# Performance work log

Measured on AMD Instinct MI355X. Metric: run time of the kernel, lower is better.

Reference implementation:

```python
import jax, jax.numpy as jnp
import numpy as np

NUM_AGENTS = 5
B = 512          # graphs in batch
NP = 50          # nodes per graph
N = B * NP
EPG = 400        # edges per graph
E = B * EPG
H, C = 8, 64     # heads, per-head channels
F = H * C        # 512 node feature dim after concat
GRU_IN = 2 * F   # agent emb + graph emb
GRU_H = 128


def _gat_layer(x, src, dst, ea, W, a_src, a_dst, We, ae, b):
    # PyG GATConv: per-edge additive attention with edge features, softmax over dst
    n = x.shape[0]
    h = (x @ W).reshape(n, H, C)                          # [n,H,C]
    al = (h * a_src).sum(-1)[src] + (h * a_dst).sum(-1)[dst] \
         + ((ea @ We).reshape(-1, H, C) * ae).sum(-1)     # [e,H]
    al = jax.nn.leaky_relu(al, 0.2)
    amax = jax.ops.segment_max(al, dst, num_segments=n)
    amax = jnp.where(jnp.isfinite(amax), amax, 0.0)
    p = jnp.exp(al - amax[dst])
    denom = jax.ops.segment_sum(p, dst, num_segments=n)
    alpha = p / (denom[dst] + 1e-16)
    out = jax.ops.segment_sum(alpha[:, :, None] * h[src], dst, num_segments=n)
    return out.reshape(n, F) + b


def _gru(x_seq, h0, Wih, Whh, bih, bhh):
    # torch nn.GRU math, batch_first input [B,T,I]
    def step(h, x_t):
        gi = x_t @ Wih + bih
        gh = h @ Whh + bhh
        ir, iz, inn = jnp.split(gi, 3, axis=-1)
        hr, hz, hn = jnp.split(gh, 3, axis=-1)
        r = jax.nn.sigmoid(ir + hr)
        z = jax.nn.sigmoid(iz + hz)
        n_ = jnp.tanh(inn + r * hn)
        h_new = (1.0 - z) * n_ + z * h
        return h_new, h_new
    h_last, ys = jax.lax.scan(step, h0, jnp.swapaxes(x_seq, 0, 1))
    return jnp.swapaxes(ys, 0, 1), h_last


def _forward(x, edge_index, edge_attr, hidden_state,
             W1, a_src1, a_dst1, We1, ae1, b1,
             W2, a_src2, a_dst2, We2, ae2, b2,
             W3, a_src3, a_dst3, We3, ae3, b3,
             gru_Wih, gru_Whh, gru_bih, gru_bhh,
             fc1_W, fc1_b, fc2_W, fc2_b, log_std):
    src, dst = edge_index[0], edge_index[1]
    # conv1: add_self_loops=False
    x1 = jax.nn.relu(_gat_layer(x, src, dst, edge_attr, W1, a_src1, a_dst1, We1, ae1, b1))
    # conv2/3: add self loops with fill_value='mean' (mean of incoming edge_attr per node)
    cnt = jax.ops.segment_sum(jnp.ones((E,), x.dtype), dst, num_segments=N)
    loop_attr = jax.ops.segment_sum(edge_attr, dst, num_segments=N) / jnp.maximum(cnt, 1.0)[:, None]
    loops = jnp.arange(N, dtype=edge_index.dtype)
    src2 = jnp.concatenate([src, loops])
    dst2 = jnp.concatenate([dst, loops])
    ea2 = jnp.concatenate([edge_attr, loop_attr], axis=0)
    x2 = jax.nn.relu(_gat_layer(x1, src2, dst2, ea2, W2, a_src2, a_dst2, We2, ae2, b2))
    x3 = jax.nn.relu(_gat_layer(x2, src2, dst2, ea2, W3, a_src3, a_dst3, We3, ae3, b3))
    # global mean pool (each graph has NP nodes, contiguous)
    batch = jnp.repeat(jnp.arange(B), NP)
    graph_emb = jax.ops.segment_sum(x3, batch, num_segments=B) / NP   # [B,F]
    # first NUM_AGENTS nodes of each graph
    agent_idx = (jnp.arange(B)[:, None] * NP + jnp.arange(NUM_AGENTS)).reshape(-1)
    agent_emb = x3[agent_idx]                                          # [B*A,F]
    graph_rep = jnp.repeat(graph_emb, NUM_AGENTS, axis=0)
    combined = jnp.concatenate([agent_emb, graph_rep], axis=1).reshape(B, NUM_AGENTS, GRU_IN)
    gru_out, h_last = _gru(combined, hidden_state[0], gru_Wih, gru_Whh, gru_bih, gru_bhh)
    f1 = jax.nn.relu(gru_out.reshape(-1, GRU_H) @ fc1_W + fc1_b)
    action_mean = (f1 @ fc2_W + fc2_b).reshape(B, NUM_AGENTS, -1)
    action_std = jnp.broadcast_to(jnp.exp(jnp.clip(log_std, -20.0, 2.0)), action_mean.shape)
    return action_mean, action_std, h_last[None]


def setup_inputs() -> dict:
    ks = jax.random.split(jax.random.key(0), 24)
    rng = np.random.default_rng(0)
    # random edges within each graph, no self-loops
    src_l = rng.integers(0, NP, size=(B, EPG))
    dst_l = (src_l + 1 + rng.integers(0, NP - 1, size=(B, EPG))) % NP
    off = (np.arange(B) * NP)[:, None]
    edge_index = jnp.asarray(np.stack([(src_l + off).reshape(-1), (dst_l + off).reshape(-1)]), dtype=jnp.int32)

    def p(k, shape, fan):
        return jax.random.normal(k, shape, jnp.float32) / float(np.sqrt(fan))

    z = lambda *s: jnp.zeros(s, jnp.float32)
    return {
        "x": jax.random.normal(ks[0], (N, 4), jnp.float32),
        "edge_index": edge_index,
        "edge_attr": jax.random.uniform(ks[1], (E, 1), jnp.float32),
        "hidden_state": z(1, B, GRU_H),
        "W1": p(ks[2], (4, F), 4), "a_src1": p(ks[3], (H, C), C), "a_dst1": p(ks[4], (H, C), C),
        "We1": p(ks[5], (1, F), 1), "ae1": p(ks[6], (H, C), C), "b1": z(F),
        "W2": p(ks[7], (F, F), F), "a_src2": p(ks[8], (H, C), C), "a_dst2": p(ks[9], (H, C), C),
        "We2": p(ks[10], (1, F), 1), "ae2": p(ks[11], (H, C), C), "b2": z(F),
        "W3": p(ks[12], (F, F), F), "a_src3": p(ks[13], (H, C), C), "a_dst3": p(ks[14], (H, C), C),
        "We3": p(ks[15], (1, F), 1), "ae3": p(ks[16], (H, C), C), "b3": z(F),
        "gru_Wih": p(ks[17], (GRU_IN, 3 * GRU_H), GRU_IN),
        "gru_Whh": p(ks[18], (GRU_H, 3 * GRU_H), GRU_H),
        "gru_bih": z(3 * GRU_H), "gru_bhh": z(3 * GRU_H),
        "fc1_W": p(ks[19], (GRU_H, 64), GRU_H), "fc1_b": z(64),
        "fc2_W": p(ks[20], (64, 3), 64), "fc2_b": z(3),
        "log_std": jnp.full((1, 1, 3), -1.6, jnp.float32),
    }


def reference(x, edge_index, edge_attr, hidden_state,
              W1, a_src1, a_dst1, We1, ae1, b1,
              W2, a_src2, a_dst2, We2, ae2, b2,
              W3, a_src3, a_dst3, We3, ae3, b3,
              gru_Wih, gru_Whh, gru_bih, gru_bhh,
              fc1_W, fc1_b, fc2_W, fc2_b, log_std):
    return _forward(x, edge_index, edge_attr, hidden_state,
                    W1, a_src1, a_dst1, We1, ae1, b1,
                    W2, a_src2, a_dst2, We2, ae2, b2,
                    W3, a_src3, a_dst3, We3, ae3, b3,
                    gru_Wih, gru_Whh, gru_bih, gru_bhh,
                    fc1_W, fc1_b, fc2_W, fc2_b, log_std)
```

## Files before the change

kernel.cpp:

```cpp
#include <hip/hip_runtime.h>
#include <math.h>

#define NN 25600
#define BB 512
#define NP 50
#define EPG 400
#define EE 204800
#define HH 8
#define FF 512
#define GRUH 128
#define GRUIN 1024

typedef unsigned short ushort_t;
typedef __attribute__((ext_vector_type(8))) short bf16x8;
typedef __attribute__((ext_vector_type(4))) float f32x4;

__device__ __forceinline__ float wave_reduce_sum(float v) {
  #pragma unroll
  for (int m = 32; m >= 1; m >>= 1) v += __shfl_xor(v, m, 64);
  return v;
}

__device__ __forceinline__ ushort_t f2bf(float x) {
  union { float f; unsigned int u; } v; v.f = x;
  unsigned int r = v.u + 0x7fffu + ((v.u >> 16) & 1u);
  return (ushort_t)(r >> 16);
}

__device__ __forceinline__ float bf2f(ushort_t u) {
  union { unsigned int u; float f; } v; v.u = ((unsigned int)u) << 16;
  return v.f;
}

__device__ __forceinline__ void gload_lds16(const ushort_t* g, ushort_t* l) {
  __builtin_amdgcn_global_load_lds(
      (const __attribute__((address_space(1))) void*)g,
      (__attribute__((address_space(3))) void*)l, 16, 0, 0);
}

__global__ __launch_bounds__(256) void k_pre(
    const float* __restrict__ W2, const float* __restrict__ W3,
    const float* __restrict__ Wih,
    ushort_t* __restrict__ w2t, ushort_t* __restrict__ w3t, ushort_t* __restrict__ wiht,
    const int* __restrict__ ei, const float* __restrict__ eattr,
    int* __restrict__ rowp, ushort_t* __restrict__ esrc, float* __restrict__ eea,
    float* __restrict__ lattr,
    const float* __restrict__ We1, const float* __restrict__ ae1,
    const float* __restrict__ We2, const float* __restrict__ ae2,
    const float* __restrict__ We3, const float* __restrict__ ae3,
    float* __restrict__ wdot) {
  int b = blockIdx.x, tid = threadIdx.x;
  __shared__ float t[32][33];
  __shared__ int cnt[NP];
  __shared__ float esum[NP];
  __shared__ int rp[NP + 1];
  __shared__ int cur[NP];

  if (b < 896) {
    const float* W; ushort_t* Wt; int K, N, n0, k0;
    if (b < 256)      { W = W2;  Wt = w2t;  K = 512;  N = 512; n0 = (b & 15) * 32;        k0 = (b >> 4) * 32; }
    else if (b < 512) { W = W3;  Wt = w3t;  K = 512;  N = 512; n0 = ((b - 256) & 15) * 32; k0 = ((b - 256) >> 4) * 32; }
    else              { W = Wih; Wt = wiht; K = 1024; N = 384; n0 = ((b - 512) % 12) * 32; k0 = ((b - 512) / 12) * 32; }
    int tx = tid & 31, ty = tid >> 5;
    #pragma unroll
    for (int i = 0; i < 4; i++)
      t[ty + i * 8][tx] = W[(size_t)(k0 + ty + i * 8) * N + n0 + tx];
    __syncthreads();
    #pragma unroll
    for (int i = 0; i < 4; i++)
      Wt[(size_t)(n0 + ty + i * 8) * K + k0 + tx] = f2bf(t[tx][ty + i * 8]);
  } else if (b < 1408) {
    int g = b - 896;
    if (tid < NP) { cnt[tid] = 0; esum[tid] = 0.f; }
    __syncthreads();
    for (int e = tid; e < EPG; e += 256) {
      int ge = g * EPG + e;
      int dl = ei[EE + ge] - g * NP;
      atomicAdd(&cnt[dl], 1);
      atomicAdd(&esum[dl], eattr[ge]);
    }
    __syncthreads();
    if (tid == 0) {
      int s = 0;
      for (int i = 0; i < NP; i++) { rp[i] = s; cur[i] = s; s += cnt[i]; }
      rp[NP] = s;
    }
    __syncthreads();
    if (tid <= NP) rowp[g * 64 + tid] = rp[tid];
    if (tid < NP) lattr[g * NP + tid] = esum[tid] / (float)max(cnt[tid], 1);
    for (int e = tid; e < EPG; e += 256) {
      int ge = g * EPG + e;
      int sl = ei[ge] - g * NP;
      int dl = ei[EE + ge] - g * NP;
      int pos = atomicAdd(&cur[dl], 1);
      esrc[g * EPG + pos] = (ushort_t)sl;
      eea[g * EPG + pos] = eattr[ge];
    }
  } else {
    int w = tid >> 6, lane = tid & 63;
    for (int i = 0; i < 6; i++) {
      int idx = w + 4 * i;
      int l = idx >> 3, h = idx & 7;
      const float* We = l == 0 ? We1 : (l == 1 ? We2 : We3);
      const float* ae = l == 0 ? ae1 : (l == 1 ? ae2 : ae3);
      float v = wave_reduce_sum(We[h * 64 + lane] * ae[h * 64 + lane]);
      if (lane == 0) wdot[l * 8 + h] = v;
    }
  }
}

__global__ __launch_bounds__(512, 4) void k_layer(
    const ushort_t* __restrict__ Xbf,
    const float* __restrict__ x4, const float* __restrict__ W1,
    const ushort_t* __restrict__ Wt,
    const float* __restrict__ a_src, const float* __restrict__ a_dst,
    ushort_t* __restrict__ xout, ushort_t* __restrict__ cbf,
    const int* __restrict__ rowp, const ushort_t* __restrict__ esrc,
    const float* __restrict__ eea, const float* __restrict__ lattr,
    const float* __restrict__ wdot_all, const float* __restrict__ bias,
    int layer, int self_loops) {
  int g = blockIdx.x, half = blockIdx.y, tid = threadIdx.x;
  int w = tid >> 6, l = tid & 63;
  int head = w & 3, fhalf = w >> 2;
  int flb = head * 64 + fhalf * 32;
  int fbase = half * 256;
  int m_l = l & 15, quad = l >> 4, rq = quad * 4, kq8 = quad * 8;

  __shared__ __align__(16) ushort_t hS[256 * 64];
  __shared__ __align__(16) ushort_t U[12800];
  __shared__ float pds[512], pdd[512];
  __shared__ float sslS[256], sdlS[256];
  __shared__ ushort_t esrcS[400];
  __shared__ float eeaS[400];
  __shared__ int rowpS[51];
  __shared__ float lattrS[50];

  for (int i = tid; i < 400; i += 512) { esrcS[i] = esrc[g * EPG + i]; eeaS[i] = eea[g * EPG + i]; }
  if (tid <= NP) rowpS[tid] = rowp[g * 64 + tid];
  if (tid < NP) lattrS[tid] = lattr[g * NP + tid];

  f32x4 acc[2][4];
  #pragma unroll
  for (int i = 0; i < 2; i++)
    #pragma unroll
    for (int j = 0; j < 4; j++) acc[i][j] = (f32x4){0.f, 0.f, 0.f, 0.f};

  if (layer == 0) {
    float* W1s = (float*)U;
    float* xs = (float*)U + 1024;
    for (int i = tid; i < 1024; i += 512)
      W1s[i] = W1[(i >> 8) * 512 + fbase + (i & 255)];
    if (tid < NP) *(float4*)(&xs[tid * 4]) = *(const float4*)(&x4[(size_t)(g * NP + tid) * 4]);
    else if (tid < 64) *(float4*)(&xs[tid * 4]) = make_float4(0.f, 0.f, 0.f, 0.f);
    __syncthreads();
    float xr[4][4];
    #pragma unroll
    for (int nt = 0; nt < 4; nt++)
      #pragma unroll
      for (int k = 0; k < 4; k++) xr[nt][k] = xs[(nt * 16 + m_l) * 4 + k];
    #pragma unroll
    for (int mt = 0; mt < 2; mt++) {
      float wv[4][4];
      #pragma unroll
      for (int r = 0; r < 4; r++)
        #pragma unroll
        for (int k = 0; k < 4; k++) wv[r][k] = W1s[k * 256 + flb + mt * 16 + rq + r];
      #pragma unroll
      for (int nt = 0; nt < 4; nt++)
        #pragma unroll
        for (int r = 0; r < 4; r++)
          acc[mt][nt][r] = xr[nt][0] * wv[r][0] + xr[nt][1] * wv[r][1]
                         + xr[nt][2] * wv[r][2] + xr[nt][3] * wv[r][3];
    }
    __syncthreads();
  } else {
    ushort_t* Bs = U;
    const ushort_t* Arow = Wt + (size_t)(fbase + flb + m_l) * FF + kq8;
    const ushort_t* Bg = Xbf + (size_t)(g * NP + w * 16 + (l >> 2)) * FF + (l & 3) * 8;
    ushort_t* BsW = U + w * 512;
    for (int k0 = 0; k0 < FF; k0 += 128) {
      if (w < 4) {
        #pragma unroll
        for (int j = 0; j < 4; j++)
          gload_lds16(Bg + k0 + j * 32, BsW + j * 2048);
      }
      __syncthreads();
      #pragma unroll
      for (int j = 0; j < 4; j++) {
        int kk = k0 + j * 32;
        bf16x8 af0 = *(const bf16x8*)(Arow + kk);
        bf16x8 af1 = *(const bf16x8*)(Arow + (size_t)16 * FF + kk);
        #pragma unroll
        for (int nt = 0; nt < 4; nt++) {
          bf16x8 bf = *(const bf16x8*)(Bs + j * 2048 + (nt * 16 + m_l) * 32 + kq8);
          acc[0][nt] = __builtin_amdgcn_mfma_f32_16x16x32_bf16(af0, bf, acc[0][nt], 0, 0, 0);
          acc[1][nt] = __builtin_amdgcn_mfma_f32_16x16x32_bf16(af1, bf, acc[1][nt], 0, 0, 0);
        }
      }
      __syncthreads();
    }
  }

  float ds[4] = {0.f, 0.f, 0.f, 0.f}, dd[4] = {0.f, 0.f, 0.f, 0.f};
  #pragma unroll
  for (int mt = 0; mt < 2; mt++) {
    float a_s[4], a_d[4];
    #pragma unroll
    for (int r = 0; r < 4; r++) {
      int fg = fbase + flb + mt * 16 + rq + r;
      a_s[r] = a_src[fg]; a_d[r] = a_dst[fg];
    }
    #pragma unroll
    for (int nt = 0; nt < 4; nt++) {
      int s = nt * 16 + m_l;
      #pragma unroll
      for (int r = 0; r < 4; r++) {
        float v = acc[mt][nt][r];
        ds[nt] += v * a_s[r];
        dd[nt] += v * a_d[r];
        int fl = flb + mt * 16 + rq + r;
        hS[fl * 64 + (s ^ (((fl >> 2) & 7) << 3))] = f2bf(v);
      }
    }
  }
  #pragma unroll
  for (int nt = 0; nt < 4; nt++) {
    ds[nt] += __shfl_xor(ds[nt], 16, 64); ds[nt] += __shfl_xor(ds[nt], 32, 64);
    dd[nt] += __shfl_xor(dd[nt], 16, 64); dd[nt] += __shfl_xor(dd[nt], 32, 64);
  }
  if (l < 16) {
    #pragma unroll
    for (int nt = 0; nt < 4; nt++) {
      pds[w * 64 + nt * 16 + l] = ds[nt];
      pdd[w * 64 + nt * 16 + l] = dd[nt];
    }
  }
  __syncthreads();

  { uint4* z = (uint4*)U; for (int i = tid; i < 1600; i += 512) z[i] = make_uint4(0u, 0u, 0u, 0u); }
  if (tid < 256) {
    sslS[tid] = pds[tid] + pds[tid + 256];
    sdlS[tid] = pdd[tid] + pdd[tid + 256];
  }
  __syncthreads();

  float wdot = wdot_all[layer * 8 + half * 4 + head];
  if (w < 4 && l < NP) {
    ushort_t* AmH = U + w * 3200;
    int d = l;
    int e0 = rowpS[d], e1 = rowpS[d + 1];
    float sd = sdlS[w * 64 + d];
    float m = -1e30f;
    for (int e = e0; e < e1; e++) {
      float al = sslS[w * 64 + esrcS[e]] + sd + eeaS[e] * wdot;
      al = al > 0.f ? al : 0.2f * al;
      m = fmaxf(m, al);
    }
    float al_loop = 0.f;
    if (self_loops) {
      al_loop = sslS[w * 64 + d] + sd + lattrS[d] * wdot;
      al_loop = al_loop > 0.f ? al_loop : 0.2f * al_loop;
      m = fmaxf(m, al_loop);
    }
    if (e1 > e0 || self_loops) {
      float denom = 0.f;
      for (int e = e0; e < e1; e++) {
        float al = sslS[w * 64 + esrcS[e]] + sd + eeaS[e] * wdot;
        al = al > 0.f ? al : 0.2f * al;
        float p = __expf(al - m);
        denom += p;
        int sp = esrcS[e] ^ ((d & 3) << 3);
        float prev = bf2f(AmH[d * 64 + sp]);
        AmH[d * 64 + sp] = f2bf(prev + p);
      }
      if (self_loops) {
        float p = __expf(al_loop - m);
        denom += p;
        int sp = d ^ ((d & 3) << 3);
        float prev = bf2f(AmH[d * 64 + sp]);
        AmH[d * 64 + sp] = f2bf(prev + p);
      }
      float inv = 1.f / (denom + 1e-16f);
      #pragma unroll
      for (int c = 0; c < 8; c++) {
        union { ushort_t u[8]; uint4 q; } pk;
        pk.q = *(uint4*)(AmH + d * 64 + c * 8);
        #pragma unroll
        for (int j = 0; j < 8; j++) pk.u[j] = f2bf(bf2f(pk.u[j]) * inv);
        *(uint4*)(AmH + d * 64 + c * 8) = pk.q;
      }
    }
  }
  __syncthreads();

  ushort_t* AmW = U + head * 3200;
  f32x4 oacc[2][4];
  #pragma unroll
  for (int i = 0; i < 2; i++)
    #pragma unroll
    for (int j = 0; j < 4; j++) oacc[i][j] = (f32x4){0.f, 0.f, 0.f, 0.f};
  #pragma unroll
  for (int kc = 0; kc < 2; kc++) {
    int kb = kc * 32 + kq8;
    bf16x8 bfr2[4];
    #pragma unroll
    for (int nt = 0; nt < 4; nt++) {
      int d = nt * 16 + m_l;
      int rd = d < NP ? d : 0;
      bfr2[nt] = *(const bf16x8*)(AmW + rd * 64 + (kb ^ ((rd & 3) << 3)));
    }
    #pragma unroll
    for (int mt = 0; mt < 2; mt++) {
      int fl = flb + mt * 16 + m_l;
      bf16x8 afr = *(const bf16x8*)(hS + fl * 64 + (kb ^ (((fl >> 2) & 7) << 3)));
      #pragma unroll
      for (int nt = 0; nt < 4; nt++)
        oacc[mt][nt] = __builtin_amdgcn_mfma_f32_16x16x32_bf16(afr, bfr2[nt], oacc[mt][nt], 0, 0, 0);
    }
  }

  float vv[2][4][4];
  #pragma unroll
  for (int mt = 0; mt < 2; mt++) {
    const float4 bv = *(const float4*)(&bias[fbase + flb + mt * 16 + rq]);
    #pragma unroll
    for (int nt = 0; nt < 4; nt++) {
      vv[mt][nt][0] = fmaxf(oacc[mt][nt][0] + bv.x, 0.f);
      vv[mt][nt][1] = fmaxf(oacc[mt][nt][1] + bv.y, 0.f);
      vv[mt][nt][2] = fmaxf(oacc[mt][nt][2] + bv.z, 0.f);
      vv[mt][nt][3] = fmaxf(oacc[mt][nt][3] + bv.w, 0.f);
    }
  }

  if (cbf == nullptr) {
    #pragma unroll
    for (int nt = 0; nt < 4; nt++) {
      int d = nt * 16 + m_l;
      if (d < NP) {
        #pragma unroll
        for (int mt = 0; mt < 2; mt++) {
          union { ushort_t u[4]; uint2 v; } pk;
          #pragma unroll
          for (int r = 0; r < 4; r++) pk.u[r] = f2bf(vv[mt][nt][r]);
          *(uint2*)(&xout[(size_t)(g * NP + d) * FF + fbase + flb + mt * 16 + rq]) = pk.v;
        }
      }
    }
  } else {
    #pragma unroll
    for (int mt = 0; mt < 2; mt++) {
      float msum[4];
      #pragma unroll
      for (int r = 0; r < 4; r++) {
        float t = 0.f;
        #pragma unroll
        for (int nt = 0; nt < 4; nt++) {
          int d = nt * 16 + m_l;
          t += (d < NP) ? vv[mt][nt][r] : 0.f;
        }
        t += __shfl_xor(t, 1, 64); t += __shfl_xor(t, 2, 64);
        t += __shfl_xor(t, 4, 64); t += __shfl_xor(t, 8, 64);
        msum[r] = t * (1.f / NP);
      }
      if (m_l == 0) {
        union { ushort_t u[4]; uint2 v; } pk;
        #pragma unroll
        for (int r = 0; r < 4; r++) pk.u[r] = f2bf(msum[r]);
        #pragma unroll
        for (int t5 = 0; t5 < 5; t5++)
          *(uint2*)(&cbf[(size_t)(g * 5 + t5) * GRUIN + 512 + fbase + flb + mt * 16 + rq]) = pk.v;
      }
      if (m_l < 5) {
        union { ushort_t u[4]; uint2 v; } pk;
        #pragma unroll
        for (int r = 0; r < 4; r++) pk.u[r] = f2bf(vv[mt][0][r]);
        *(uint2*)(&cbf[(size_t)(g * 5 + m_l) * GRUIN + fbase + flb + mt * 16 + rq]) = pk.v;
      }
    }
  }
}

__global__ __launch_bounds__(256) void k_bgemm(
    const ushort_t* __restrict__ A, const ushort_t* __restrict__ Bt,
    const float* __restrict__ bias, float* __restrict__ C,
    int M, int N, int K) {
  __shared__ ushort_t As[128 * 32];
  __shared__ ushort_t Bs[128 * 32];
  int tid = threadIdx.x;
  int w = tid >> 6, l = tid & 63;
  int row0 = blockIdx.y * 128, col0 = blockIdx.x * 128;
  int wr = w >> 1, wc = w & 1;

  f32x4 acc[4][4];
  #pragma unroll
  for (int i = 0; i < 4; i++)
    #pragma unroll
    for (int j = 0; j < 4; j++) acc[i][j] = (f32x4){0.f, 0.f, 0.f, 0.f};

  int srow = w * 32 + (l >> 2);
  int skcol = (l & 3) * 8;
  const ushort_t* Ag = A + (size_t)(row0 + srow) * K + skcol;
  const ushort_t* Bg = Bt + (size_t)(col0 + srow) * K + skcol;
  ushort_t* AsW = &As[w * 1024];
  ushort_t* BsW = &Bs[w * 1024];

  int m_l = l & 15, kq = (l >> 4) * 8;
  const ushort_t* ArdA = &As[(wr * 64 + m_l) * 32 + kq];
  const ushort_t* BrdB = &Bs[(wc * 64 + m_l) * 32 + kq];

  for (int k0 = 0; k0 < K; k0 += 32) {
    gload_lds16(Ag + k0, AsW);
    gload_lds16(Ag + (size_t)16 * K + k0, AsW + 512);
    gload_lds16(Bg + k0, BsW);
    gload_lds16(Bg + (size_t)16 * K + k0, BsW + 512);
    __syncthreads();
    bf16x8 af[4], bfr[4];
    #pragma unroll
    for (int t = 0; t < 4; t++) {
      af[t]  = *(const bf16x8*)(ArdA + t * 16 * 32);
      bfr[t] = *(const bf16x8*)(BrdB + t * 16 * 32);
    }
    #pragma unroll
    for (int mt = 0; mt < 4; mt++)
      #pragma unroll
      for (int nt = 0; nt < 4; nt++)
        acc[mt][nt] = __builtin_amdgcn_mfma_f32_16x16x32_bf16(af[mt], bfr[nt], acc[mt][nt], 0, 0, 0);
    __syncthreads();
  }

  int cl = l & 15, rq = (l >> 4) * 4;
  #pragma unroll
  for (int mt = 0; mt < 4; mt++) {
    #pragma unroll
    for (int nt = 0; nt < 4; nt++) {
      int col = col0 + wc * 64 + nt * 16 + cl;
      float bv = bias ? bias[col] : 0.f;
      #pragma unroll
      for (int r = 0; r < 4; r++) {
        int row = row0 + wr * 64 + mt * 16 + rq + r;
        C[(size_t)row * N + col] = acc[mt][nt][r] + bv;
      }
    }
  }
}

__global__ void k_grufc(const float* __restrict__ gi_all, const float* __restrict__ h0,
                        const float* __restrict__ Whh, const float* __restrict__ bhh,
                        const float* __restrict__ fc1W, const float* __restrict__ fc1b,
                        const float* __restrict__ fc2W, const float* __restrict__ fc2b,
                        const float* __restrict__ log_std, float* __restrict__ dout) {
  int b = blockIdx.x, tid = threadIdx.x;
  __shared__ float hl[GRUH];
  __shared__ float ghb[384];
  __shared__ float go[5 * GRUH];
  __shared__ float f1[5 * 64];
  if (tid < GRUH) hl[tid] = h0[b * GRUH + tid];
  for (int t = 0; t < 5; t++) {
    __syncthreads();
    float acc = bhh[tid];
    for (int k = 0; k < GRUH; k++) acc += hl[k] * Whh[k * 384 + tid];
    ghb[tid] = acc;
    __syncthreads();
    if (tid < GRUH) {
      const float* gi = gi_all + (size_t)(b * 5 + t) * 384;
      float r = 1.f / (1.f + expf(-(gi[tid] + ghb[tid])));
      float z = 1.f / (1.f + expf(-(gi[128 + tid] + ghb[128 + tid])));
      float nn = tanhf(gi[256 + tid] + r * ghb[256 + tid]);
      float hn = (1.f - z) * nn + z * hl[tid];
      go[t * GRUH + tid] = hn;
      hl[tid] = hn;
    }
  }
  __syncthreads();
  if (tid < GRUH) dout[15360 + b * GRUH + tid] = hl[tid];
  if (tid < 320) {
    int t = tid >> 6, j = tid & 63;
    float acc = fc1b[j];
    for (int k = 0; k < GRUH; k++) acc += go[t * GRUH + k] * fc1W[k * 64 + j];
    f1[t * 64 + j] = fmaxf(acc, 0.f);
  }
  __syncthreads();
  if (tid < 15) {
    int t = tid / 3, o = tid % 3;
    float v = fc2b[o];
    for (int j = 0; j < 64; j++) v += f1[t * 64 + j] * fc2W[j * 3 + o];
    dout[(b * 5 + t) * 3 + o] = v;
    float ls = log_std[o];
    ls = fminf(fmaxf(ls, -20.f), 2.f);
    dout[7680 + (b * 5 + t) * 3 + o] = expf(ls);
  }
}

extern "C" void kernel_launch(void* const* d_in, const int* in_sizes, int n_in,
                              void* d_out, int out_size, void* d_ws, size_t ws_size,
                              hipStream_t stream) {
  const float* x      = (const float*)d_in[0];
  const int*   ei     = (const int*)d_in[1];
  const float* eattr  = (const float*)d_in[2];
  const float* hstate = (const float*)d_in[3];
  const float* W1  = (const float*)d_in[4];
  const float* as1 = (const float*)d_in[5];
  const float* ad1 = (const float*)d_in[6];
  const float* We1 = (const float*)d_in[7];
  const float* ae1 = (const float*)d_in[8];
  const float* b1  = (const float*)d_in[9];
  const float* W2  = (const float*)d_in[10];
  const float* as2 = (const float*)d_in[11];
  const float* ad2 = (const float*)d_in[12];
  const float* We2 = (const float*)d_in[13];
  const float* ae2 = (const float*)d_in[14];
  const float* b2  = (const float*)d_in[15];
  const float* W3  = (const float*)d_in[16];
  const float* as3 = (const float*)d_in[17];
  const float* ad3 = (const float*)d_in[18];
  const float* We3 = (const float*)d_in[19];
  const float* ae3 = (const float*)d_in[20];
  const float* b3  = (const float*)d_in[21];
  const float* Wih = (const float*)d_in[22];
  const float* Whh = (const float*)d_in[23];
  const float* bih = (const float*)d_in[24];
  const float* bhh = (const float*)d_in[25];
  const float* fc1W = (const float*)d_in[26];
  const float* fc1b = (const float*)d_in[27];
  const float* fc2W = (const float*)d_in[28];
  const float* fc2b = (const float*)d_in[29];
  const float* lstd = (const float*)d_in[30];

  float* ws = (float*)d_ws;
  ushort_t* xbf1 = (ushort_t*)ws;
  ushort_t* xbf2 = (ushort_t*)(ws + 6569984);
  float* p = ws + 2 * 6569984;
  int*   rowp  = (int*)p;         p += 32768;
  ushort_t* esrc = (ushort_t*)p;  p += 102400;
  float* eea   = p;               p += 204800;
  float* lattr = p;               p += 25600;
  float* wdot  = p;               p += 32;
  ushort_t* w2t  = (ushort_t*)p;  p += 131072;
  ushort_t* w3t  = (ushort_t*)p;  p += 131072;
  ushort_t* wiht = (ushort_t*)p;  p += 196608;
  ushort_t* cbf  = (ushort_t*)p;  p += 1310720;
  float* gi_all  = p;             p += 983040;
  float* dout = (float*)d_out;

  k_pre<<<1409, 256, 0, stream>>>(W2, W3, Wih, w2t, w3t, wiht, ei, eattr,
                                  rowp, esrc, eea, lattr,
                                  We1, ae1, We2, ae2, We3, ae3, wdot);

  k_layer<<<dim3(BB, 2), 512, 0, stream>>>(nullptr, x, W1, nullptr, as1, ad1,
                                           xbf1, nullptr, rowp, esrc, eea, lattr,
                                           wdot, b1, 0, 0);
  k_layer<<<dim3(BB, 2), 512, 0, stream>>>(xbf1, nullptr, nullptr, w2t, as2, ad2,
                                           xbf2, nullptr, rowp, esrc, eea, lattr,
                                           wdot, b2, 1, 1);
  k_layer<<<dim3(BB, 2), 512, 0, stream>>>(xbf2, nullptr, nullptr, w3t, as3, ad3,
                                           nullptr, cbf, rowp, esrc, eea, lattr,
                                           wdot, b3, 2, 1);

  k_bgemm<<<dim3(3, 20), 256, 0, stream>>>(cbf, wiht, bih, gi_all, 2560, 384, GRUIN);

  k_grufc<<<BB, 384, 0, stream>>>(gi_all, hstate, Whh, bhh, fc1W, fc1b,
                                  fc2W, fc2b, lstd, dout);
}
```

Baseline: 318.8 us.

## Stage weight tiles in LDS for projection GEMM and pad h layout

The projection GEMM for layers 2-3 now stages both the transposed weight tile and the node-feature tile into shared memory with async global-to-LDS loads over 64-wide K chunks, using all 8 waves for loading. Previously weight fragments were read straight from global memory per lane. The h tile moves from an XOR-swizzled layout to a row-padded layout (stride 72), and the bf16 results are written as packed 32-bit pairs exchanged across neighbouring lanes. The aim is fewer scattered global reads and LDS bank conflicts, in exchange for more shared memory per block, which may lower occupancy.

Measured after the change: 319.7 us. No clear change (+0.3%).

```diff
diff --git a/kernel.cpp b/kernel.cpp
--- a/kernel.cpp
+++ b/kernel.cpp
@@ -121,13 +121,13 @@
     int layer, int self_loops) {
   int g = blockIdx.x, half = blockIdx.y, tid = threadIdx.x;
   int w = tid >> 6, l = tid & 63;
-  int head = w & 3, fhalf = w >> 2;
-  int flb = head * 64 + fhalf * 32;
+  int head = w & 3;
+  int flb = head * 64 + (w >> 2) * 32;
   int fbase = half * 256;
   int m_l = l & 15, quad = l >> 4, rq = quad * 4, kq8 = quad * 8;
 
-  __shared__ __align__(16) ushort_t hS[256 * 64];
-  __shared__ __align__(16) ushort_t U[12800];
+  __shared__ __align__(16) ushort_t hS[256 * 72];
+  __shared__ __align__(16) ushort_t AmU[12800];
   __shared__ float pds[512], pdd[512];
   __shared__ float sslS[256], sdlS[256];
   __shared__ ushort_t esrcS[400];
@@ -146,8 +146,8 @@
     for (int j = 0; j < 4; j++) acc[i][j] = (f32x4){0.f, 0.f, 0.f, 0.f};
 
   if (layer == 0) {
-    float* W1s = (float*)U;
-    float* xs = (float*)U + 1024;
+    float* W1s = (float*)AmU;
+    float* xs = (float*)AmU + 1024;
     for (int i = tid; i < 1024; i += 512)
       W1s[i] = W1[(i >> 8) * 512 + fbase + (i & 255)];
     if (tid < NP) *(float4*)(&xs[tid * 4]) = *(const float4*)(&x4[(size_t)(g * NP + tid) * 4]);
@@ -174,27 +174,29 @@
     }
     __syncthreads();
   } else {
-    ushort_t* Bs = U;
-    const ushort_t* Arow = Wt + (size_t)(fbase + flb + m_l) * FF + kq8;
-    const ushort_t* Bg = Xbf + (size_t)(g * NP + w * 16 + (l >> 2)) * FF + (l & 3) * 8;
-    ushort_t* BsW = U + w * 512;
-    for (int k0 = 0; k0 < FF; k0 += 128) {
-      if (w < 4) {
-        #pragma unroll
-        for (int j = 0; j < 4; j++)
-          gload_lds16(Bg + k0 + j * 32, BsW + j * 2048);
-      }
+    ushort_t* hA = hS;
+    ushort_t* hB = AmU;
+    int arow = (l >> 3), acol = (l & 7) * 8;
+    for (int k0 = 0; k0 < FF; k0 += 64) {
+      #pragma unroll
+      for (int j = 0; j < 4; j++)
+        gload_lds16(Wt + (size_t)(fbase + w * 32 + j * 8 + arow) * FF + k0 + acol,
+                    hA + w * 2048 + j * 512);
+      gload_lds16(Xbf + (size_t)(g * NP + w * 8 + arow) * FF + k0 + acol,
+                  hB + w * 512);
       __syncthreads();
       #pragma unroll
-      for (int j = 0; j < 4; j++) {
-        int kk = k0 + j * 32;
-        bf16x8 af0 = *(const bf16x8*)(Arow + kk);
-        bf16x8 af1 = *(const bf16x8*)(Arow + (size_t)16 * FF + kk);
-        #pragma unroll
-        for (int nt = 0; nt < 4; nt++) {
-          bf16x8 bf = *(const bf16x8*)(Bs + j * 2048 + (nt * 16 + m_l) * 32 + kq8);
-          acc[0][nt] = __builtin_amdgcn_mfma_f32_16x16x32_bf16(af0, bf, acc[0][nt], 0, 0, 0);
-          acc[1][nt] = __builtin_amdgcn_mfma_f32_16x16x32_bf16(af1, bf, acc[1][nt], 0, 0, 0);
+      for (int kc = 0; kc < 2; kc++) {
+        bf16x8 bfr[4];
+        #pragma unroll
+        for (int nt = 0; nt < 4; nt++)
+          bfr[nt] = *(const bf16x8*)(hB + (nt * 16 + m_l) * 64 + kc * 32 + kq8);
+        #pragma unroll
+        for (int mt = 0; mt < 2; mt++) {
+          bf16x8 af = *(const bf16x8*)(hA + (flb + mt * 16 + m_l) * 64 + kc * 32 + kq8);
+          #pragma unroll
+          for (int nt = 0; nt < 4; nt++)
+            acc[mt][nt] = __builtin_amdgcn_mfma_f32_16x16x32_bf16(af, bfr[nt], acc[mt][nt], 0, 0, 0);
         }
       }
       __syncthreads();
@@ -202,6 +204,7 @@
   }
 
   float ds[4] = {0.f, 0.f, 0.f, 0.f}, dd[4] = {0.f, 0.f, 0.f, 0.f};
+  int rbase = (m_l & 1) * 2;
   #pragma unroll
   for (int mt = 0; mt < 2; mt++) {
     float a_s[4], a_d[4];
@@ -212,15 +215,20 @@
     }
     #pragma unroll
     for (int nt = 0; nt < 4; nt++) {
-      int s = nt * 16 + m_l;
+      unsigned int pk[4];
       #pragma unroll
       for (int r = 0; r < 4; r++) {
         float v = acc[mt][nt][r];
         ds[nt] += v * a_s[r];
         dd[nt] += v * a_d[r];
-        int fl = flb + mt * 16 + rq + r;
-        hS[fl * 64 + (s ^ (((fl >> 2) & 7) << 3))] = f2bf(v);
-      }
+        float o = __shfl_xor(v, 1, 64);
+        unsigned int own = f2bf(v), oth = f2bf(o);
+        pk[r] = (m_l & 1) ? (oth | (own << 16)) : (own | (oth << 16));
+      }
+      int col = nt * 16 + (m_l & ~1);
+      int row0 = flb + mt * 16 + rq + rbase;
+      *(unsigned int*)(&hS[row0 * 72 + col]) = pk[rbase];
+      *(unsigned int*)(&hS[(row0 + 1) * 72 + col]) = pk[rbase + 1];
     }
   }
   #pragma unroll
@@ -237,7 +245,7 @@
   }
   __syncthreads();
 
-  { uint4* z = (uint4*)U; for (int i = tid; i < 1600; i += 512) z[i] = make_uint4(0u, 0u, 0u, 0u); }
+  { uint4* z = (uint4*)AmU; for (int i = tid; i < 1600; i += 512) z[i] = make_uint4(0u, 0u, 0u, 0u); }
   if (tid < 256) {
     sslS[tid] = pds[tid] + pds[tid + 256];
     sdlS[tid] = pdd[tid] + pdd[tid + 256];
@@ -246,7 +254,7 @@
 
   float wdot = wdot_all[layer * 8 + half * 4 + head];
   if (w < 4 && l < NP) {
-    ushort_t* AmH = U + w * 3200;
+    ushort_t* AmH = AmU + w * 3200;
     int d = l;
     int e0 = rowpS[d], e1 = rowpS[d + 1];
     float sd = sdlS[w * 64 + d];
@@ -293,7 +301,7 @@
   }
   __syncthreads();
 
-  ushort_t* AmW = U + head * 3200;
+  ushort_t* AmW = AmU + head * 3200;
   f32x4 oacc[2][4];
   #pragma unroll
   for (int i = 0; i < 2; i++)
@@ -312,7 +320,7 @@
     #pragma unroll
     for (int mt = 0; mt < 2; mt++) {
       int fl = flb + mt * 16 + m_l;
-      bf16x8 afr = *(const bf16x8*)(hS + fl * 64 + (kb ^ (((fl >> 2) & 7) << 3)));
+      bf16x8 afr = *(const bf16x8*)(&hS[fl * 72 + kb]);
       #pragma unroll
       for (int nt = 0; nt < 4; nt++)
         oacc[mt][nt] = __builtin_amdgcn_mfma_f32_16x16x32_bf16(afr, bfr2[nt], oacc[mt][nt], 0, 0, 0);
```
